# Kernel optimization log

Hardware: AMD Instinct MI355X
Metric: run time of the kernel (lower is better)

Reference implementation:

```python
import jax, jax.numpy as jnp
import numpy as np

C = 256
RED = 2
C2 = C // RED


def setup_inputs() -> dict:
    key = jax.random.key(0)
    ks = jax.random.split(key, 6)
    B, H, W = 8, 64, 64
    x = jax.random.normal(ks[0], (B, C, H, W), dtype=jnp.float32)
    # 1x1 convs stored as [out_ch, in_ch] matrices
    W1 = jax.random.normal(ks[1], (C2, C), dtype=jnp.float32) * (1.0 / np.sqrt(C))
    b1 = jax.random.normal(ks[2], (C2,), dtype=jnp.float32) * 0.01
    W2 = jax.random.normal(ks[3], (C, C2), dtype=jnp.float32) * (1.0 / np.sqrt(C2))
    b2 = jax.random.normal(ks[4], (C,), dtype=jnp.float32) * 0.01
    # torch inits scale to zeros; use randn so the residual branch is active
    scale = jax.random.normal(ks[5], (1, C, 1, 1), dtype=jnp.float32)
    return {"x": x, "W1": W1, "b1": b1, "W2": W2, "b2": b2, "scale": scale}


def reference(x, W1, b1, W2, b2, scale):
    B, Cc, H, Wd = x.shape
    # conv1 (1x1): [B,C,H,W] -> [B,C2,H,W]
    y = jnp.einsum('bchw,oc->bohw', x, W1) + b1[None, :, None, None]
    # flatten spatial, move channels last: [B, N, C2]
    y = y.reshape(B, C2, H * Wd).transpose(0, 2, 1)
    # unscaled self-attention over N spatial positions
    att = jax.nn.softmax(jnp.einsum('bmc,bnc->bmn', y, y), axis=-1)  # [B,N,N]
    out = jnp.einsum('bmn,bnc->bmc', att, y)  # [B,N,C2]
    # faithful to torch: raw .view(B,-1,H,W) WITHOUT permuting back
    out = out.reshape(B, C2, H, Wd)
    # conv2 (1x1): [B,C2,H,W] -> [B,C,H,W]
    out = jnp.einsum('bchw,oc->bohw', out, W2) + b2[None, :, None, None]
    return out * scale + x
```

## Files before the change

kernel.cpp:

```cpp
#include <hip/hip_runtime.h>

#define B_  8
#define C_  256
#define C2_ 128
#define N_  4096
#define LOG2E 1.44269504088896f

typedef _Float16 f16;
typedef _Float16 f16x4 __attribute__((ext_vector_type(4)));
typedef _Float16 f16x8 __attribute__((ext_vector_type(8)));
typedef float f32x4  __attribute__((ext_vector_type(4)));

static __device__ __forceinline__ unsigned pk2(float a, float b) {
  return __builtin_bit_cast(unsigned, __builtin_amdgcn_cvt_pkrtz(a, b));
}

static __device__ __forceinline__ void plane16_swap(unsigned a, unsigned b,
                                                    unsigned& r0, unsigned& r1) {
#if __has_builtin(__builtin_amdgcn_permlane16_swap)
  auto r = __builtin_amdgcn_permlane16_swap(a, b, false, false);
  r0 = (unsigned)r[0]; r1 = (unsigned)r[1];
#else
  asm volatile("v_permlane16_swap_b32 %0, %1" : "+v"(a), "+v"(b));
  r0 = a; r1 = b;
#endif
}

static __device__ __forceinline__ void gload16(const void* g, void* l) {
  __builtin_amdgcn_global_load_lds(
      (const __attribute__((address_space(1))) unsigned int*)g,
      (__attribute__((address_space(3))) unsigned int*)l, 16, 0, 0);
}

__global__ __launch_bounds__(256)
void prep_kernel(const float* __restrict__ W1, const float* __restrict__ W2,
                 f16* __restrict__ w1h, f16* __restrict__ w2h)
{
  int i = blockIdx.x * 256 + threadIdx.x;
  w1h[i] = (f16)W1[i];
  w2h[i] = (f16)W2[i];
}

__global__ __launch_bounds__(256, 3)
void conv1_kernel(const float* __restrict__ x,
                  const f16* __restrict__ w1h,
                  const float* __restrict__ b1,
                  f16* __restrict__ Y, f16* __restrict__ Yt)
{
  __shared__ __align__(16) char smem[32768];
  f16* Xh = (f16*)smem;
  f16* Ah = (f16*)(smem + 16384);
  f16* T  = (f16*)smem;

  const int t = threadIdx.x;
  const int w = t >> 6, lane = t & 63, quad = lane >> 4, l16 = lane & 15;
  const int b = blockIdx.x, nt0 = blockIdx.y;

#pragma unroll
  for (int pass = 0; pass < 8; pass++) {
    int c  = (t >> 3) + pass * 32;
    int n4 = t & 7;
    float4 v = *(const float4*)(x + ((long)(b * C_ + c)) * N_ + nt0 * 32 + n4 * 4);
    f16x4 h = {(f16)v.x, (f16)v.y, (f16)v.z, (f16)v.w};
    *(f16x4*)(&Xh[c * 32 + (n4 ^ (c & 7)) * 4]) = h;
  }
  __syncthreads();
#pragma unroll
  for (int pass = 0; pass < 4; pass++) {
    int n  = t & 31;
    int kb = (t >> 5) + pass * 8;
    f16x8 vh;
#pragma unroll
    for (int jj = 0; jj < 8; jj++) {
      int cc = kb * 8 + jj;
      vh[jj] = Xh[cc * 32 + ((n >> 2) ^ (cc & 7)) * 4 + (n & 3)];
    }
    *(f16x8*)(&Ah[n * 256 + (kb ^ (n & 7)) * 8]) = vh;
  }
  __syncthreads();

  f16x8 bh[2][8];
#pragma unroll
  for (int nt = 0; nt < 2; nt++) {
    int c2 = w * 32 + nt * 16 + l16;
#pragma unroll
    for (int ks = 0; ks < 8; ks++)
      bh[nt][ks] = *(const f16x8*)(w1h + c2 * C_ + ks * 32 + quad * 8);
  }

  f32x4 acc[2][2];
#pragma unroll
  for (int i = 0; i < 2; i++)
#pragma unroll
    for (int j = 0; j < 2; j++) acc[i][j] = (f32x4){0.f, 0.f, 0.f, 0.f};

#pragma unroll
  for (int ks = 0; ks < 8; ks++)
#pragma unroll
    for (int mt = 0; mt < 2; mt++) {
      f16x8 ah = *(const f16x8*)(&Ah[(mt * 16 + l16) * 256 + (((ks * 4 + quad) ^ (l16 & 7))) * 8]);
#pragma unroll
      for (int nt = 0; nt < 2; nt++)
        acc[mt][nt] = __builtin_amdgcn_mfma_f32_16x16x32_f16(ah, bh[nt][ks], acc[mt][nt], 0, 0, 0);
    }
  __syncthreads();

#pragma unroll
  for (int nt = 0; nt < 2; nt++) {
    int c2 = w * 32 + nt * 16 + l16;
    float bv = b1[c2];
#pragma unroll
    for (int mt = 0; mt < 2; mt++)
#pragma unroll
      for (int rg = 0; rg < 4; rg++) {
        int n = mt * 16 + quad * 4 + rg;
        T[c2 * 40 + n] = (f16)(acc[mt][nt][rg] + bv);
      }
  }
  __syncthreads();
#pragma unroll
  for (int pass = 0; pass < 2; pass++) {
    int r  = (t >> 2) + pass * 64;
    int c8 = (t & 3) * 8;
    f16x8 v = *(const f16x8*)(&T[r * 40 + c8]);
    *(f16x8*)(Yt + ((long)(b * C2_ + r)) * N_ + nt0 * 32 + c8) = v;
  }
#pragma unroll
  for (int pass = 0; pass < 2; pass++) {
    int row = t & 31;
    int cg  = (t >> 5) + pass * 8;
    f16x8 v;
#pragma unroll
    for (int jj = 0; jj < 8; jj++) v[jj] = T[(cg * 8 + jj) * 40 + row];
    *(f16x8*)(Y + ((long)(b * N_ + nt0 * 32 + row)) * C2_ + cg * 8) = v;
  }
}

__global__ __launch_bounds__(256, 2)
void attn_kernel(const f16* __restrict__ Y, const f16* __restrict__ Yt,
                 f16* __restrict__ Op, float* __restrict__ ls)
{
  __shared__ f16 Ks[2][64 * 128];
  __shared__ f16 Vs[2][128 * 64];
  __shared__ float nsqf[128];

  const int t = threadIdx.x;
  const int w = t >> 6, lane = t & 63, quad = lane >> 4, l16 = lane & 15;
  const int b = blockIdx.x, qt = blockIdx.y, s = blockIdx.z;
  const int ns = gridDim.z;
  const f16* Yb  = Y  + (long)b * N_ * C2_;
  const f16* Ytb = Yt + (long)b * C2_ * N_;
  const int g0 = (s * 64) / ns;
  const int g1 = ((s + 1) * 64) / ns;
  const int nt_ = g1 - g0;

  int koff[4], voff[4];
#pragma unroll
  for (int i = 0; i < 4; i++) {
    int p = w + 4 * i;
    int r = 4 * p + (lane >> 4);
    koff[i] = r * C2_ + ((l16 ^ (r & 15)) * 8);
    int d = 8 * p + (lane >> 3);
    voff[i] = d * N_ + (((lane & 7) ^ (d & 7)) * 8);
  }

  f16x8 qf[2][4];
#pragma unroll
  for (int mt = 0; mt < 2; mt++)
#pragma unroll
    for (int ks = 0; ks < 4; ks++)
      qf[mt][ks] = *(const f16x8*)(Yb + (long)(qt * 128 + w * 32 + mt * 16 + l16) * C2_ + ks * 32 + quad * 8);

  {
    int r = t >> 1, half = t & 1;
    float ss = 0.f;
#pragma unroll
    for (int j = 0; j < 8; j++) {
      f16x8 v = *(const f16x8*)(Yb + (long)(qt * 128 + r) * C2_ + half * 64 + j * 8);
#pragma unroll
      for (int e = 0; e < 8; e++) { float f = (float)v[e]; ss = fmaf(f, f, ss); }
    }
    ss += __shfl_xor(ss, 1);
    if (!half) nsqf[r] = ss;
  }

  {
    const f16* gk = Yb + (long)(g0 * 64) * C2_;
#pragma unroll
    for (int i = 0; i < 4; i++)
      gload16(gk + koff[i], &Ks[0][(w + 4 * i) * 512]);
  }
  __syncthreads();

  float nm[2];
  nm[0] = nsqf[w * 32 + l16] * LOG2E;
  nm[1] = nsqf[w * 32 + 16 + l16] * LOG2E;

  f16x8 ones8;
#pragma unroll
  for (int j = 0; j < 8; j++) ones8[j] = (f16)1.0f;

  f32x4 Oa[2][8];
#pragma unroll
  for (int i = 0; i < 2; i++)
#pragma unroll
    for (int j = 0; j < 8; j++) Oa[i][j] = (f32x4){0.f, 0.f, 0.f, 0.f};
  f32x4 lac[2] = {(f32x4){0.f,0.f,0.f,0.f}, (f32x4){0.f,0.f,0.f,0.f}};

  f16x8 pa_prev[2][2];

#pragma unroll 1
  for (int i = 0; i < nt_; i++) {
    const int g = g0 + i;
    const int kb = i & 1;

    if (i + 1 < nt_) {
      const f16* gk = Yb + (long)((g + 1) * 64) * C2_;
#pragma unroll
      for (int j = 0; j < 4; j++)
        gload16(gk + koff[j], &Ks[kb ^ 1][(w + 4 * j) * 512]);
    }
    {
      const f16* gv = Ytb + g * 64;
#pragma unroll
      for (int j = 0; j < 4; j++)
        gload16(gv + voff[j], &Vs[kb][(w + 4 * j) * 512]);
    }

    f32x4 S[4][2];
#pragma unroll
    for (int a = 0; a < 4; a++)
#pragma unroll
      for (int j = 0; j < 2; j++) S[a][j] = (f32x4){0.f, 0.f, 0.f, 0.f};
#pragma unroll
    for (int ks = 0; ks < 4; ks++) {
      f16x8 bfr[4];
#pragma unroll
      for (int nt = 0; nt < 4; nt++)
        bfr[nt] = *(const f16x8*)(&Ks[kb][(nt * 16 + l16) * 128 + (((ks * 4 + quad) ^ l16)) * 8]);
      __builtin_amdgcn_s_setprio(1);
#pragma unroll
      for (int nt = 0; nt < 4; nt++)
#pragma unroll
        for (int mt = 0; mt < 2; mt++)
          S[nt][mt] = __builtin_amdgcn_mfma_f32_16x16x32_f16(bfr[nt], qf[mt][ks], S[nt][mt], 0, 0, 0);
      __builtin_amdgcn_s_setprio(0);
    }

    if (i > 0) {
#pragma unroll
      for (int ks2 = 0; ks2 < 2; ks2++) {
        f16x8 vb[8];
#pragma unroll
        for (int dt = 0; dt < 8; dt++)
          vb[dt] = *(const f16x8*)(&Vs[kb ^ 1][(dt * 16 + l16) * 64 + (((ks2 * 4 + quad) ^ (l16 & 7))) * 8]);
        __builtin_amdgcn_s_setprio(1);
#pragma unroll
        for (int mt = 0; mt < 2; mt++) {
#pragma unroll
          for (int dt = 0; dt < 8; dt++)
            Oa[mt][dt] = __builtin_amdgcn_mfma_f32_16x16x32_f16(pa_prev[ks2][mt], vb[dt], Oa[mt][dt], 0, 0, 0);
          lac[mt] = __builtin_amdgcn_mfma_f32_16x16x32_f16(pa_prev[ks2][mt], ones8, lac[mt], 0, 0, 0);
        }
        __builtin_amdgcn_s_setprio(0);
      }
    }

#pragma unroll
    for (int ks2 = 0; ks2 < 2; ks2++)
#pragma unroll
      for (int mt = 0; mt < 2; mt++) {
        float n0 = nm[mt];
        unsigned xa0 = pk2(exp2f(fminf(fmaf(S[2 * ks2][mt][0], LOG2E, -n0), 11.0f)),
                           exp2f(fminf(fmaf(S[2 * ks2][mt][1], LOG2E, -n0), 11.0f)));
        unsigned xa1 = pk2(exp2f(fminf(fmaf(S[2 * ks2][mt][2], LOG2E, -n0), 11.0f)),
                           exp2f(fminf(fmaf(S[2 * ks2][mt][3], LOG2E, -n0), 11.0f)));
        unsigned xb0 = pk2(exp2f(fminf(fmaf(S[2 * ks2 + 1][mt][0], LOG2E, -n0), 11.0f)),
                           exp2f(fminf(fmaf(S[2 * ks2 + 1][mt][1], LOG2E, -n0), 11.0f)));
        unsigned xb1 = pk2(exp2f(fminf(fmaf(S[2 * ks2 + 1][mt][2], LOG2E, -n0), 11.0f)),
                           exp2f(fminf(fmaf(S[2 * ks2 + 1][mt][3], LOG2E, -n0), 11.0f)));
        union { unsigned u[4]; f16x8 v; } P;
        {
          auto c = __builtin_amdgcn_permlane32_swap(xa0, xb0, false, false);
          plane16_swap((unsigned)c[0], (unsigned)c[1], P.u[0], P.u[2]);
        }
        {
          auto c = __builtin_amdgcn_permlane32_swap(xa1, xb1, false, false);
          plane16_swap((unsigned)c[0], (unsigned)c[1], P.u[1], P.u[3]);
        }
        pa_prev[ks2][mt] = P.v;
      }

    __syncthreads();
  }

  {
    const int kb = (nt_ - 1) & 1;
#pragma unroll
    for (int ks2 = 0; ks2 < 2; ks2++) {
      f16x8 vb[8];
#pragma unroll
      for (int dt = 0; dt < 8; dt++)
        vb[dt] = *(const f16x8*)(&Vs[kb][(dt * 16 + l16) * 64 + (((ks2 * 4 + quad) ^ (l16 & 7))) * 8]);
#pragma unroll
      for (int mt = 0; mt < 2; mt++) {
#pragma unroll
        for (int dt = 0; dt < 8; dt++)
          Oa[mt][dt] = __builtin_amdgcn_mfma_f32_16x16x32_f16(pa_prev[ks2][mt], vb[dt], Oa[mt][dt], 0, 0, 0);
        lac[mt] = __builtin_amdgcn_mfma_f32_16x16x32_f16(pa_prev[ks2][mt], ones8, lac[mt], 0, 0, 0);
      }
    }
  }

  const long rbase = ((long)s * B_ + b) * N_ + qt * 128;
#pragma unroll
  for (int mt = 0; mt < 2; mt++)
#pragma unroll
    for (int rg = 0; rg < 4; rg++) {
      int r = w * 32 + mt * 16 + quad * 4 + rg;
#pragma unroll
      for (int dt = 0; dt < 8; dt++)
        Op[(rbase + r) * C2_ + dt * 16 + l16] = (f16)Oa[mt][dt][rg];
      if (l16 == 0) ls[rbase + r] = lac[mt][rg];
    }
}

__global__ __launch_bounds__(256, 2)
void conv2_kernel(const f16* __restrict__ Op, const float* __restrict__ ls,
                  const f16* __restrict__ w2h,
                  const float* __restrict__ b2,
                  const float* __restrict__ scale,
                  const float* __restrict__ x,
                  float* __restrict__ out, int ns)
{
  __shared__ __align__(16) char smem2[70144];
  f16*   Or   = (f16*)smem2;
  f16*   Bsw  = (f16*)(smem2 + 18432);
  float* invL = (float*)(smem2 + 34816);
  float* Obuf = (float*)(smem2 + 35328);

  const int t = threadIdx.x;
  const int w = t >> 6, lane = t & 63, quad = lane >> 4, l16 = lane & 15;
  const int b = blockIdx.x, pt = blockIdx.y;
  const long base0 = (long)b * 524288;

  if (t < 128) {
    int q = t * 32 + (pt >> 1);
    float l = 0.f;
    for (int si = 0; si < ns; si++)
      l += ls[(long)si * 32768 + (long)b * N_ + q];
    invL[t] = 1.0f / fmaxf(l, 1e-20f);
  }
  __syncthreads();

#pragma unroll
  for (int pass = 0; pass < 4; pass++) {
    int j = (t >> 3) + pass * 32;
    int c8 = (t & 7) * 8;
    float fa[8] = {0.f,0.f,0.f,0.f,0.f,0.f,0.f,0.f};
    for (int si = 0; si < ns; si++) {
      f16x8 a = *(const f16x8*)(Op + (long)si * 4194304 + base0 + (long)j * N_ + pt * 64 + c8);
#pragma unroll
      for (int jj = 0; jj < 8; jj++) fa[jj] += (float)a[jj];
    }
    float iv = invL[j];
    f16x8 r;
#pragma unroll
    for (int jj = 0; jj < 8; jj++)
      r[jj] = (f16)(fa[jj] * iv);
    *(f16x8*)(&Or[j * 72 + c8]) = r;
  }
  __syncthreads();
#pragma unroll
  for (int pass = 0; pass < 4; pass++) {
    int p = t & 63;
    int q = (t >> 6) + pass * 4;
    f16x8 vv;
#pragma unroll
    for (int jj = 0; jj < 8; jj++) vv[jj] = Or[(q * 8 + jj) * 72 + p];
    *(f16x8*)(&Bsw[p * 128 + ((q ^ (p & 15))) * 8]) = vv;
  }
  __syncthreads();

#pragma unroll 1
  for (int oh = 0; oh < 2; oh++) {
    f32x4 acc[2][4];
#pragma unroll
    for (int i = 0; i < 2; i++)
#pragma unroll
      for (int j = 0; j < 4; j++) acc[i][j] = (f32x4){0.f, 0.f, 0.f, 0.f};

#pragma unroll
    for (int ks = 0; ks < 4; ks++) {
      f16x8 bfr[4];
#pragma unroll
      for (int nt = 0; nt < 4; nt++)
        bfr[nt] = *(const f16x8*)(&Bsw[(nt * 16 + l16) * 128 + (((ks * 4 + quad) ^ l16)) * 8]);
#pragma unroll
      for (int mt = 0; mt < 2; mt++) {
        int o = oh * 128 + w * 32 + mt * 16 + l16;
        f16x8 ah = *(const f16x8*)(w2h + o * C2_ + ks * 32 + quad * 8);
#pragma unroll
        for (int nt = 0; nt < 4; nt++)
          acc[mt][nt] = __builtin_amdgcn_mfma_f32_16x16x32_f16(ah, bfr[nt], acc[mt][nt], 0, 0, 0);
      }
    }

    __syncthreads();
#pragma unroll
    for (int mt = 0; mt < 2; mt++)
#pragma unroll
      for (int nt = 0; nt < 4; nt++)
#pragma unroll
        for (int rg = 0; rg < 4; rg++)
          Obuf[(w * 32 + mt * 16 + quad * 4 + rg) * 68 + nt * 16 + l16] = acc[mt][nt][rg];
    __syncthreads();
#pragma unroll
    for (int pass = 0; pass < 8; pass++) {
      int idx = pass * 256 + t;
      int ol  = idx >> 4;
      int p4  = (idx & 15) * 4;
      float4 v = *(const float4*)(&Obuf[ol * 68 + p4]);
      int o = oh * 128 + ol;
      float so = scale[o], bo = b2[o];
      long xo = ((long)b * C_ + o) * N_ + pt * 64 + p4;
      float4 xv = *(const float4*)(x + xo);
      float4 r;
      r.x = (v.x + bo) * so + xv.x;
      r.y = (v.y + bo) * so + xv.y;
      r.z = (v.z + bo) * so + xv.z;
      r.w = (v.w + bo) * so + xv.w;
      *(float4*)(out + xo) = r;
    }
  }
}

extern "C" void kernel_launch(void* const* d_in, const int* in_sizes, int n_in,
                              void* d_out, int out_size, void* d_ws, size_t ws_size,
                              hipStream_t stream) {
  const float* x     = (const float*)d_in[0];
  const float* W1    = (const float*)d_in[1];
  const float* b1    = (const float*)d_in[2];
  const float* W2    = (const float*)d_in[3];
  const float* b2    = (const float*)d_in[4];
  const float* scale = (const float*)d_in[5];
  float* outp = (float*)d_out;

  const size_t NE = (size_t)B_ * N_ * C2_;
  const int ns = 2;

  f16* Y   = (f16*)d_ws;
  f16* Yt  = Y + NE;
  f16* Op  = Yt + NE;
  float* ls = (float*)(Op + (size_t)ns * NE);
  f16* w1h = (f16*)(ls + (size_t)ns * 32768);
  f16* w2h = w1h + 32768;

  prep_kernel <<<dim3(128),       dim3(256), 0, stream>>>(W1, W2, w1h, w2h);
  conv1_kernel<<<dim3(8, 128),    dim3(256), 0, stream>>>(x, w1h, b1, Y, Yt);
  attn_kernel <<<dim3(8, 32, ns), dim3(256), 0, stream>>>(Y, Yt, Op, ls);
  conv2_kernel<<<dim3(8, 64),     dim3(256), 0, stream>>>(Op, ls, w2h, b2, scale, x, outp, ns);
}
```

Baseline: 197.8 us.

## Drop weight prep kernel and split conv2 output halves across grid

Removes the separate fp16 weight-conversion kernel; conv1 and conv2 now load fp32 weights and convert them in registers. conv2 gets a third grid dimension over the two output-channel halves instead of looping over them. Obuf now aliases the start of shared memory, which halves LDS use and lets the launch bound rise to 4 blocks. The cost is that each conv2 block still does the full Op reduction and transpose, so that work is duplicated across the two halves, and weight loads now read twice the bytes.

Measured after the change: 207.7 us. +5.0%, slower.

```diff
diff --git a/kernel.cpp b/kernel.cpp
--- a/kernel.cpp
+++ b/kernel.cpp
@@ -32,18 +32,17 @@
       (__attribute__((address_space(3))) unsigned int*)l, 16, 0, 0);
 }
 
-__global__ __launch_bounds__(256)
-void prep_kernel(const float* __restrict__ W1, const float* __restrict__ W2,
-                 f16* __restrict__ w1h, f16* __restrict__ w2h)
-{
-  int i = blockIdx.x * 256 + threadIdx.x;
-  w1h[i] = (f16)W1[i];
-  w2h[i] = (f16)W2[i];
+static __device__ __forceinline__ f16x8 ld_cvt8(const float* p) {
+  float4 a = *(const float4*)(p);
+  float4 b = *(const float4*)(p + 4);
+  f16x8 h = {(f16)a.x, (f16)a.y, (f16)a.z, (f16)a.w,
+             (f16)b.x, (f16)b.y, (f16)b.z, (f16)b.w};
+  return h;
 }
 
 __global__ __launch_bounds__(256, 3)
 void conv1_kernel(const float* __restrict__ x,
-                  const f16* __restrict__ w1h,
+                  const float* __restrict__ W1,
                   const float* __restrict__ b1,
                   f16* __restrict__ Y, f16* __restrict__ Yt)
 {
@@ -85,7 +84,7 @@
     int c2 = w * 32 + nt * 16 + l16;
 #pragma unroll
     for (int ks = 0; ks < 8; ks++)
-      bh[nt][ks] = *(const f16x8*)(w1h + c2 * C_ + ks * 32 + quad * 8);
+      bh[nt][ks] = ld_cvt8(W1 + c2 * C_ + ks * 32 + quad * 8);
   }
 
   f32x4 acc[2][2];
@@ -325,23 +324,23 @@
     }
 }
 
-__global__ __launch_bounds__(256, 2)
+__global__ __launch_bounds__(256, 4)
 void conv2_kernel(const f16* __restrict__ Op, const float* __restrict__ ls,
-                  const f16* __restrict__ w2h,
+                  const float* __restrict__ W2,
                   const float* __restrict__ b2,
                   const float* __restrict__ scale,
                   const float* __restrict__ x,
                   float* __restrict__ out, int ns)
 {
-  __shared__ __align__(16) char smem2[70144];
+  __shared__ __align__(16) char smem2[35328];
   f16*   Or   = (f16*)smem2;
   f16*   Bsw  = (f16*)(smem2 + 18432);
   float* invL = (float*)(smem2 + 34816);
-  float* Obuf = (float*)(smem2 + 35328);
+  float* Obuf = (float*)smem2;
 
   const int t = threadIdx.x;
   const int w = t >> 6, lane = t & 63, quad = lane >> 4, l16 = lane & 15;
-  const int b = blockIdx.x, pt = blockIdx.y;
+  const int b = blockIdx.x, pt = blockIdx.y, oh = blockIdx.z;
   const long base0 = (long)b * 524288;
 
   if (t < 128) {
@@ -382,56 +381,53 @@
   }
   __syncthreads();
 
-#pragma unroll 1
-  for (int oh = 0; oh < 2; oh++) {
-    f32x4 acc[2][4];
-#pragma unroll
-    for (int i = 0; i < 2; i++)
-#pragma unroll
-      for (int j = 0; j < 4; j++) acc[i][j] = (f32x4){0.f, 0.f, 0.f, 0.f};
-
-#pragma unroll
-    for (int ks = 0; ks < 4; ks++) {
-      f16x8 bfr[4];
+  f32x4 acc[2][4];
+#pragma unroll
+  for (int i = 0; i < 2; i++)
+#pragma unroll
+    for (int j = 0; j < 4; j++) acc[i][j] = (f32x4){0.f, 0.f, 0.f, 0.f};
+
+#pragma unroll
+  for (int ks = 0; ks < 4; ks++) {
+    f16x8 bfr[4];
+#pragma unroll
+    for (int nt = 0; nt < 4; nt++)
+      bfr[nt] = *(const f16x8*)(&Bsw[(nt * 16 + l16) * 128 + (((ks * 4 + quad) ^ l16)) * 8]);
+#pragma unroll
+    for (int mt = 0; mt < 2; mt++) {
+      int o = oh * 128 + w * 32 + mt * 16 + l16;
+      f16x8 ah = ld_cvt8(W2 + o * C2_ + ks * 32 + quad * 8);
 #pragma unroll
       for (int nt = 0; nt < 4; nt++)
-        bfr[nt] = *(const f16x8*)(&Bsw[(nt * 16 + l16) * 128 + (((ks * 4 + quad) ^ l16)) * 8]);
-#pragma unroll
-      for (int mt = 0; mt < 2; mt++) {
-        int o = oh * 128 + w * 32 + mt * 16 + l16;
-        f16x8 ah = *(const f16x8*)(w2h + o * C2_ + ks * 32 + quad * 8);
-#pragma unroll
-        for (int nt = 0; nt < 4; nt++)
-          acc[mt][nt] = __builtin_amdgcn_mfma_f32_16x16x32_f16(ah, bfr[nt], acc[mt][nt], 0, 0, 0);
-      }
-    }
-
-    __syncthreads();
-#pragma unroll
-    for (int mt = 0; mt < 2; mt++)
-#pragma unroll
-      for (int nt = 0; nt < 4; nt++)
-#pragma unroll
-        for (int rg = 0; rg < 4; rg++)
-          Obuf[(w * 32 + mt * 16 + quad * 4 + rg) * 68 + nt * 16 + l16] = acc[mt][nt][rg];
-    __syncthreads();
-#pragma unroll
-    for (int pass = 0; pass < 8; pass++) {
-      int idx = pass * 256 + t;
-      int ol  = idx >> 4;
-      int p4  = (idx & 15) * 4;
-      float4 v = *(const float4*)(&Obuf[ol * 68 + p4]);
-      int o = oh * 128 + ol;
-      float so = scale[o], bo = b2[o];
-      long xo = ((long)b * C_ + o) * N_ + pt * 64 + p4;
-      float4 xv = *(const float4*)(x + xo);
-      float4 r;
-      r.x = (v.x + bo) * so + xv.x;
-      r.y = (v.y + bo) * so + xv.y;
-      r.z = (v.z + bo) * so + xv.z;
-      r.w = (v.w + bo) * so + xv.w;
-      *(float4*)(out + xo) = r;
-    }
+        acc[mt][nt] = __builtin_amdgcn_mfma_f32_16x16x32_f16(ah, bfr[nt], acc[mt][nt], 0, 0, 0);
+    }
+  }
+
+  __syncthreads();
+#pragma unroll
+  for (int mt = 0; mt < 2; mt++)
+#pragma unroll
+    for (int nt = 0; nt < 4; nt++)
+#pragma unroll
+      for (int rg = 0; rg < 4; rg++)
+        Obuf[(w * 32 + mt * 16 + quad * 4 + rg) * 68 + nt * 16 + l16] = acc[mt][nt][rg];
+  __syncthreads();
+#pragma unroll
+  for (int pass = 0; pass < 8; pass++) {
+    int idx = pass * 256 + t;
+    int ol  = idx >> 4;
+    int p4  = (idx & 15) * 4;
+    float4 v = *(const float4*)(&Obuf[ol * 68 + p4]);
+    int o = oh * 128 + ol;
+    float so = scale[o], bo = b2[o];
+    long xo = ((long)b * C_ + o) * N_ + pt * 64 + p4;
+    float4 xv = *(const float4*)(x + xo);
+    float4 r;
+    r.x = (v.x + bo) * so + xv.x;
+    r.y = (v.y + bo) * so + xv.y;
+    r.z = (v.z + bo) * so + xv.z;
+    r.w = (v.w + bo) * so + xv.w;
+    *(float4*)(out + xo) = r;
   }
 }
 
@@ -453,11 +449,8 @@
   f16* Yt  = Y + NE;
   f16* Op  = Yt + NE;
   float* ls = (float*)(Op + (size_t)ns * NE);
-  f16* w1h = (f16*)(ls + (size_t)ns * 32768);
-  f16* w2h = w1h + 32768;
-
-  prep_kernel <<<dim3(128),       dim3(256), 0, stream>>>(W1, W2, w1h, w2h);
-  conv1_kernel<<<dim3(8, 128),    dim3(256), 0, stream>>>(x, w1h, b1, Y, Yt);
+
+  conv1_kernel<<<dim3(8, 128),    dim3(256), 0, stream>>>(x, W1, b1, Y, Yt);
   attn_kernel <<<dim3(8, 32, ns), dim3(256), 0, stream>>>(Y, Yt, Op, ls);
-  conv2_kernel<<<dim3(8, 64),     dim3(256), 0, stream>>>(Op, ls, w2h, b2, scale, x, outp, ns);
-}
+  conv2_kernel<<<dim3(8, 64, 2),  dim3(256), 0, stream>>>(Op, ls, W2, b2, scale, x, outp, ns);
+}
```
